# Kernel tuning notes

Hardware: AMD Instinct MI355X
Metric: run time of the kernel (lower is better)

## Reference

```python
import jax, jax.numpy as jnp
import numpy as np

BIT = 64
N_CLASS = 100
NUM_TRAIN = 100000
BATCH = 512
MU = 1.0   # config['mu']
M = 1.0    # config['m']
ETA = 0.5  # config['eta']
VUL = 1.0  # config['vul']
NTA = 1.0  # config['nta']


def setup_inputs() -> dict:
    key = jax.random.key(0)
    k1, k2, k3, k4, k5, k6 = jax.random.split(key, 6)
    u = jax.random.normal(k1, (BATCH, BIT), jnp.float32)
    # y / Y are one-hot label matrices in DFH; build realistic one-hot floats
    labels = jax.random.randint(k2, (BATCH,), 0, N_CLASS)
    y = jax.nn.one_hot(labels, N_CLASS, dtype=jnp.float32)
    ind = jax.random.randint(k3, (BATCH,), 0, NUM_TRAIN)
    U = jax.random.normal(k4, (BIT, NUM_TRAIN), jnp.float32)
    train_labels = jax.random.randint(k5, (NUM_TRAIN,), 0, N_CLASS)
    Y = jax.nn.one_hot(train_labels, N_CLASS, dtype=jnp.float32).T  # [n_class, num_train]
    V = jax.random.normal(k6, (BIT, N_CLASS), jnp.float32)
    return {"u": u, "y": y, "ind": ind, "U": U, "Y": Y, "V": V}


def _center_gradient(V, y, b):
    # 200-step gradient descent on V minimizing intra + vul*inter + nta*quant.
    n_class = V.shape[1]
    TK = V.shape[0] * (2.0 * jnp.eye(n_class, dtype=V.dtype)
                       - jnp.ones((n_class, n_class), V.dtype))
    yt = y.T  # [n_class, batch]

    def inner_loss(Vc):
        intra = jnp.mean((Vc @ yt - b) ** 2)
        inter = jnp.mean((Vc.T @ Vc - TK) ** 2)
        quant = jnp.mean((Vc - jnp.sign(Vc)) ** 2)
        return intra + VUL * inter + NTA * quant

    grad_fn = jax.grad(inner_loss)

    def step(Vc, i):
        # torch code multiplies alpha by 0.1 *before* the update at i==149 and i==179
        alpha = 0.03 * jnp.where(i >= 149, 0.1, 1.0) * jnp.where(i >= 179, 0.1, 1.0)
        return Vc - alpha * grad_fn(Vc), None

    V_new, _ = jax.lax.scan(step, V, jnp.arange(200))
    return V_new


def reference(u, y, ind, U, Y, V):
    # state buffer updates (torch: self.U[:, ind] = u.t().data, etc.)
    U = U.at[:, ind].set(u.T)
    Y = Y.at[:, ind].set(y.T)
    C = jnp.sign(V)
    b = jnp.sign(MU * (C @ y.T) + u.T)                     # [bit, batch]
    V_new = _center_gradient(V, y, b)                      # updated self.V
    s = (y @ Y > 0).astype(u.dtype)                        # [batch, num_train]
    ip = jnp.clip(0.5 * (u @ U), -100.0, 50.0)             # [batch, num_train]
    metric_loss = jnp.mean((1.0 - s) * jnp.log1p(jnp.exp(M + ip))
                           + s * jnp.log1p(jnp.exp(M - ip)))
    quantization_loss = jnp.mean((b - u.T) ** 2)
    loss = metric_loss + ETA * quantization_loss
    return loss, V_new
```

## Files before the change

### kernel.cpp

```cpp
#include <hip/hip_runtime.h>

#define BIT 64
#define NCLASS 100
#define NTRAIN 100000
#define BATCH 512

#define O_OWNER   0
#define O_LAB     200000
#define O_BMAT    200512
#define O_BSUM    233280
#define O_COUNT   239680
#define O_QSUM    239780
#define O_MSUM    239782

typedef __attribute__((ext_vector_type(8))) short short8v;
typedef __attribute__((ext_vector_type(4))) float f32x4;
typedef unsigned short ushortT;

__device__ __forceinline__ float signf(float x) {
    return (x > 0.f) ? 1.f : ((x < 0.f) ? -1.f : 0.f);
}

__device__ __forceinline__ unsigned cvtpk(float lo, float hi) {
    unsigned r;
    asm("v_cvt_pk_bf16_f32 %0, %1, %2" : "=v"(r) : "v"(lo), "v"(hi));
    return r;
}
__device__ __forceinline__ float dpp_x1(float x) {
    union { float f; int i; } v; v.f = x;
    v.i = __builtin_amdgcn_mov_dpp(v.i, 0xB1, 0xF, 0xF, false);
    return v.f;
}
__device__ __forceinline__ float dpp_x2(float x) {
    union { float f; int i; } v; v.f = x;
    v.i = __builtin_amdgcn_mov_dpp(v.i, 0x4E, 0xF, 0xF, false);
    return v.f;
}

__global__ void k_prep(const float* __restrict__ y, const int* __restrict__ ind,
                       int* owner, int* lab) {
    int b = threadIdx.x;
    const float* row = y + b * NCLASS;
    int best = 0;
    for (int c = 0; c < NCLASS; ++c)
        if (row[c] > 0.5f) best = c;
    lab[b] = best;
    atomicMax(&owner[ind[b]], b);
}

__global__ void k_b(const float* __restrict__ u, const float* __restrict__ V,
                    const int* __restrict__ lab, float* bmat, double* qsum) {
    int bb = threadIdx.x;
    int r  = blockIdx.x;
    int c = lab[bb];
    float v  = V[r * NCLASS + c];
    float uu = u[bb * BIT + r];
    float t  = signf(v) + uu;
    float bv = signf(t);
    bmat[r * BATCH + bb] = bv;
    float d = bv - uu;
    double q = (double)(d * d);
    for (int off = 32; off; off >>= 1) q += __shfl_down(q, off);
    __shared__ double wsum[8];
    int wid = threadIdx.x >> 6, lane = threadIdx.x & 63;
    if (lane == 0) wsum[wid] = q;
    __syncthreads();
    if (threadIdx.x == 0) {
        double s = 0;
        for (int w = 0; w < 8; ++w) s += wsum[w];
        atomicAdd(qsum, s);
    }
}

__global__ void k_bsum(const float* __restrict__ bmat, const int* __restrict__ lab,
                       float* Bsum, float* count) {
    __shared__ int slab[BATCH];
    for (int i = threadIdx.x; i < BATCH; i += blockDim.x) slab[i] = lab[i];
    __syncthreads();
    int idx = blockIdx.x * blockDim.x + threadIdx.x;
    if (idx < BIT * NCLASS) {
        int r = idx / NCLASS, c = idx % NCLASS;
        const float* br = bmat + r * BATCH;
        float s = 0.f;
        for (int bb = 0; bb < BATCH; ++bb)
            if (slab[bb] == c) s += br[bb];
        Bsum[idx] = s;
    }
    if (blockIdx.x == 0 && threadIdx.x < NCLASS) {
        int c = threadIdx.x, n = 0;
        for (int bb = 0; bb < BATCH; ++bb)
            if (slab[bb] == c) ++n;
        count[c] = (float)n;
    }
}

__global__ __launch_bounds__(512, 4) void k_main(
        const float* __restrict__ V, const float* __restrict__ Bsum,
        const float* __restrict__ count, const float* __restrict__ u,
        const float* __restrict__ U, const float* __restrict__ Y,
        const int* __restrict__ lab, const int* __restrict__ owner,
        double* msum, float* __restrict__ out) {
    __shared__ __align__(16) char smem[69888];

    if (blockIdx.x == 0) {
        ushortT* SAb = (ushortT*)smem;
        ushortT* SBb = (ushortT*)(smem + 32768);
        ushortT* SMf = (ushortT*)(smem + 61440);
        float*   rs  = (float*)(smem + 69632);

        const int t = threadIdx.x, l = t & 63, w = t >> 6;
        const int g = l >> 4, c16 = l & 15;
        const int h = w >> 2;
        const int mtile = w & 3;
        const int m = mtile * 16 + c16;
        const bool dg = ((mtile >> 1) == h);
        const short8v ONES = {0x3F80,0x3F80,0x3F80,0x3F80,
                              0x3F80,0x3F80,0x3F80,0x3F80};

        for (int i = t; i < 16384; i += 512) SAb[i] = 0;
        for (int i = t; i < 14336; i += 512) SBb[i] = 0;

        const float ci = 2.0f / 32768.0f;
        const float ce = 4.0f / 10000.0f;
        const float cq = 2.0f / 6400.0f;
        const float ce64 = 64.0f * ce;

        bool live[4];
        int sbO[4];
        float vreg[4][4], Kc[4][4], ncib[4][4];
        #pragma unroll
        for (int q = 0; q < 4; ++q) {
            const int nt = 4 * h + q;
            const int n0 = nt * 16 + 4 * g;
            const bool wact = (nt < 7);
            live[q] = wact && (n0 < NCLASS);
            sbO[q] = ((nt * 2 + (mtile >> 1)) * 64 +
                      (16 * (c16 >> 2) + 4 * g + (c16 & 3))) * 8 + 4 * (mtile & 1);
            #pragma unroll
            for (int r = 0; r < 4; ++r) {
                float v = 0.f, bs = 0.f, cn = 0.f;
                if (live[q]) {
                    const int n = n0 + r;
                    v  = V[m * NCLASS + n];
                    bs = Bsum[m * NCLASS + n];
                    cn = count[n];
                }
                vreg[q][r] = v;
                Kc[q][r]   = ci * cn + cq - 128.f * ce;
                ncib[q][r] = -ci * bs;
            }
        }
        const int saO0 = (mtile * 4 + 2 * h) * 512 + l * 8;
        const int saO1 = saO0 + 512;

        auto store_frags = [&](ushortT* SAn, ushortT* SBn) {
            uint4 wa;
            wa.x = cvtpk(vreg[0][0], vreg[0][1]);
            wa.y = cvtpk(vreg[0][2], vreg[0][3]);
            wa.z = cvtpk(vreg[1][0], vreg[1][1]);
            wa.w = cvtpk(vreg[1][2], vreg[1][3]);
            *(uint4*)&SAn[saO0] = wa;
            wa.x = cvtpk(vreg[2][0], vreg[2][1]);
            wa.y = cvtpk(vreg[2][2], vreg[2][3]);
            wa.z = cvtpk(vreg[3][0], vreg[3][1]);
            wa.w = cvtpk(vreg[3][2], vreg[3][3]);
            *(uint4*)&SAn[saO1] = wa;
            #pragma unroll
            for (int q = 0; q < 4; ++q) {
                if (4 * h + q < 7) {
                    float a0 = vreg[q][0], a1 = vreg[q][1];
                    float a2 = vreg[q][2], a3 = vreg[q][3];
                    float t0 = dpp_x1(a1), t1 = dpp_x1(a0);
                    float t2 = dpp_x1(a3), t3 = dpp_x1(a2);
                    const bool o1 = (l & 1);
                    float c0 = o1 ? t0 : a0;
                    float c1 = o1 ? a1 : t1;
                    float c2 = o1 ? t2 : a2;
                    float c3 = o1 ? a3 : t3;
                    float u0 = dpp_x2(c2), u1 = dpp_x2(c3);
                    float u2 = dpp_x2(c0), u3 = dpp_x2(c1);
                    const bool o2 = (l & 2);
                    float d0 = o2 ? u0 : c0;
                    float d1 = o2 ? u1 : c1;
                    float d2 = o2 ? c2 : u2;
                    float d3 = o2 ? c3 : u3;
                    uint2 wb;
                    wb.x = cvtpk(d0, d1);
                    wb.y = cvtpk(d2, d3);
                    *(uint2*)&SBn[sbO[q]] = wb;
                }
            }
        };

        __syncthreads();
        store_frags(SAb, SBb);
        __syncthreads();

        int cur = 0;
        for (int step = 0; step < 200; ++step) {
            float alpha = 0.03f;
            if (step >= 149) alpha *= 0.1f;
            if (step >= 179) alpha *= 0.1f;

            const ushortT* SAc = SAb + cur * 8192;

            f32x4 aM0 = {0.f,0.f,0.f,0.f}, aM1 = {0.f,0.f,0.f,0.f};
            f32x4 aR  = {0.f,0.f,0.f,0.f};
            #pragma unroll
            for (int ks = 0; ks < 4; ++ks) {
                short8v b  = *(const short8v*)&SAc[mtile * 2048 + ks * 512 + l * 8];
                short8v a0 = *(const short8v*)&SAc[(2 * h) * 2048 + ks * 512 + l * 8];
                short8v a1 = *(const short8v*)&SAc[(2 * h + 1) * 2048 + ks * 512 + l * 8];
                aM0 = __builtin_amdgcn_mfma_f32_16x16x32_bf16(a0, b, aM0, 0, 0, 0);
                aM1 = __builtin_amdgcn_mfma_f32_16x16x32_bf16(a1, b, aM1, 0, 0, 0);
                if (dg)
                    aR = __builtin_amdgcn_mfma_f32_16x16x32_bf16(b, ONES, aR, 0, 0, 0);
            }
            {
                uint4 sm;
                sm.x = cvtpk(aM0[0], aM0[1]);
                sm.y = cvtpk(aM0[2], aM0[3]);
                sm.z = cvtpk(aM1[0], aM1[1]);
                sm.w = cvtpk(aM1[2], aM1[3]);
                *(uint4*)&SMf[(mtile * 2 + h) * 512 + l * 8] = sm;
            }
            if (dg && c16 == 0)
                *(f32x4*)&rs[mtile * 16 + 4 * g] = aR;
            __syncthreads();

            const ushortT* SBc = SBb + cur * 7168;
            f32x4 p[4];
            #pragma unroll
            for (int q = 0; q < 4; ++q) p[q] = (f32x4){0.f,0.f,0.f,0.f};
            #pragma unroll
            for (int kb = 0; kb < 2; ++kb) {
                short8v bP = *(const short8v*)&SMf[(mtile * 2 + kb) * 512 + l * 8];
                #pragma unroll
                for (int q = 0; q < 4; ++q) {
                    if (4 * h + q < 7) {
                        short8v aP = *(const short8v*)
                            &SBc[((4 * h + q) * 2 + kb) * 512 + l * 8];
                        p[q] = __builtin_amdgcn_mfma_f32_16x16x32_bf16(aP, bP, p[q], 0, 0, 0);
                    }
                }
            }
            const float rsm = rs[m];

            #pragma unroll
            for (int q = 0; q < 4; ++q) {
                if (4 * h + q < 7) {
                    #pragma unroll
                    for (int r = 0; r < 4; ++r) {
                        const float v = vreg[q][r];
                        float t1 = __builtin_fmaf(Kc[q][r], v, ncib[q][r]);
                        t1 = __builtin_fmaf(ce,   p[q][r], t1);
                        t1 = __builtin_fmaf(ce64, rsm,     t1);
                        t1 -= __builtin_copysignf(cq, v);
                        float vn = __builtin_fmaf(-alpha, t1, v);
                        vreg[q][r] = live[q] ? vn : 0.f;
                    }
                }
            }
            store_frags(SAb + (cur ^ 1) * 8192, SBb + (cur ^ 1) * 7168);
            __syncthreads();
            cur ^= 1;
        }

        #pragma unroll
        for (int q = 0; q < 4; ++q) {
            if (live[q]) {
                const int n0 = (4 * h + q) * 16 + 4 * g;
                #pragma unroll
                for (int r = 0; r < 4; ++r)
                    out[1 + m * NCLASS + n0 + r] = vreg[q][r];
            }
        }
    } else {
        float*  ut   = (float*)smem;
        int*    slab = (int*)(smem + 34816);
        double* wsum = (double*)(smem + 36864);
        int*    tls  = (int*)(smem + 36928);

        const int t = threadIdx.x;
        const int jj = t & 255;
        const int j = (blockIdx.x - 1) * 256 + jj;
        const int half = t >> 8;
        const bool jok = (j < NTRAIN);
        slab[t] = lab[t];

        if (half == 0) {
            int tl = 0;
            if (jok) {
                for (int c = 0; c < NCLASS; ++c)
                    if (Y[(size_t)c * NTRAIN + j] > 0.5f) tl = c;
                int ow = owner[j];
                if (ow >= 0) tl = lab[ow];
            }
            tls[jj] = tl;
        }
        __syncthreads();
        const int tl = tls[jj];

        const float* colbase = U;
        size_t cstride = NTRAIN;
        if (jok) {
            int ow = owner[j];
            if (ow >= 0) { colbase = u + (size_t)ow * BIT; cstride = 1; }
            else         { colbase = U + j; }
        }

        float lsum = 0.f;
        for (int ch = 0; ch < 4; ++ch) {
            __syncthreads();
            for (int i = t; i < 8192; i += 512) {
                int buf = i >> 12, k = (i >> 6) & 63, r = i & 63;
                ut[buf * 4352 + r * 68 + k] = u[((buf * 4 + ch) * 64 + k) * BIT + r];
            }
            __syncthreads();

            if (jok) {
                const float* myut = ut + half * 4352;
                float acc[64];
                #pragma unroll
                for (int k = 0; k < 64; ++k) acc[k] = 0.f;
                #pragma unroll 2
                for (int r = 0; r < BIT; ++r) {
                    float Uv = colbase[(size_t)r * cstride];
                    const float* urow = &myut[r * 68];
                    #pragma unroll
                    for (int qq = 0; qq < 16; ++qq) {
                        float4 uv = *(const float4*)&urow[qq * 4];
                        acc[4 * qq + 0] += uv.x * Uv;
                        acc[4 * qq + 1] += uv.y * Uv;
                        acc[4 * qq + 2] += uv.z * Uv;
                        acc[4 * qq + 3] += uv.w * Uv;
                    }
                }
                const int b0 = (half * 4 + ch) * 64;
                #pragma unroll
                for (int k = 0; k < 64; ++k) {
                    float ip = fminf(fmaxf(0.5f * acc[k], -100.f), 50.f);
                    float x = (slab[b0 + k] == tl) ? (1.0f - ip) : (1.0f + ip);
                    lsum += fmaxf(x, 0.f) + __logf(1.f + __expf(-fabsf(x)));
                }
            }
        }

        double d = (double)lsum;
        for (int off = 32; off; off >>= 1) d += __shfl_down(d, off);
        const int wid = t >> 6, lane = t & 63;
        if (lane == 0) wsum[wid] = d;
        __syncthreads();
        if (t == 0) {
            double s = 0;
            for (int ww = 0; ww < 8; ++ww) s += wsum[ww];
            atomicAdd(msum, s);
        }
    }
}

__global__ void k_final(const double* __restrict__ msum,
                        const double* __restrict__ qsum, float* out) {
    if (threadIdx.x == 0) {
        double loss = (*msum) / ((double)BATCH * (double)NTRAIN)
                    + 0.5 * ((*qsum) / ((double)BIT * (double)BATCH));
        out[0] = (float)loss;
    }
}

extern "C" void kernel_launch(void* const* d_in, const int* in_sizes, int n_in,
                              void* d_out, int out_size, void* d_ws, size_t ws_size,
                              hipStream_t stream) {
    const float* u   = (const float*)d_in[0];
    const float* y   = (const float*)d_in[1];
    const int*   ind = (const int*)d_in[2];
    const float* U   = (const float*)d_in[3];
    const float* Y   = (const float*)d_in[4];
    const float* V   = (const float*)d_in[5];
    float* out = (float*)d_out;

    int*   wsI = (int*)d_ws;
    float* wsF = (float*)d_ws;
    int*   owner = wsI + O_OWNER;
    int*   lab   = wsI + O_LAB;
    float* bmat  = wsF + O_BMAT;
    float* Bsum  = wsF + O_BSUM;
    float* count = wsF + O_COUNT;
    double* qsum = (double*)(wsF + O_QSUM);
    double* msum = (double*)(wsF + O_MSUM);

    hipMemsetAsync(owner, 0xFF, NTRAIN * sizeof(int), stream);
    hipMemsetAsync(wsF + O_QSUM, 0, 4 * sizeof(float), stream);

    k_prep<<<1, 512, 0, stream>>>(y, ind, owner, lab);
    k_b<<<64, 512, 0, stream>>>(u, V, lab, bmat, qsum);
    k_bsum<<<25, 256, 0, stream>>>(bmat, lab, Bsum, count);
    k_main<<<1 + (NTRAIN + 255) / 256, 512, 0, stream>>>(
        V, Bsum, count, u, U, Y, lab, owner, msum, out);
    k_final<<<1, 64, 0, stream>>>(msum, qsum, out);
}
```

Baseline: 392.3 us.

## Fuse prep kernels and reuse register fragments in center-gradient loop

```diff
diff --git a/kernel.cpp b/kernel.cpp
--- a/kernel.cpp
+++ b/kernel.cpp
@@ -7,7 +7,6 @@
 
 #define O_OWNER   0
 #define O_LAB     200000
-#define O_BMAT    200512
 #define O_BSUM    233280
 #define O_COUNT   239680
 #define O_QSUM    239780
@@ -37,70 +36,61 @@
     return v.f;
 }
 
-__global__ void k_prep(const float* __restrict__ y, const int* __restrict__ ind,
-                       int* owner, int* lab) {
-    int b = threadIdx.x;
-    const float* row = y + b * NCLASS;
+__global__ __launch_bounds__(512) void k_pre(
+        const float* __restrict__ y, const int* __restrict__ ind,
+        const float* __restrict__ u, const float* __restrict__ V,
+        int* owner, int* lab, float* Bsum, float* count, double* qsum) {
+    __shared__ float srow[BATCH];
+    __shared__ int   labl[BATCH];
+    __shared__ double wq[8];
+    const int r = blockIdx.x;
+    const int bb = threadIdx.x;
+
+    const float* yrow = y + bb * NCLASS;
     int best = 0;
     for (int c = 0; c < NCLASS; ++c)
-        if (row[c] > 0.5f) best = c;
-    lab[b] = best;
-    atomicMax(&owner[ind[b]], b);
-}
-
-__global__ void k_b(const float* __restrict__ u, const float* __restrict__ V,
-                    const int* __restrict__ lab, float* bmat, double* qsum) {
-    int bb = threadIdx.x;
-    int r  = blockIdx.x;
-    int c = lab[bb];
-    float v  = V[r * NCLASS + c];
-    float uu = u[bb * BIT + r];
-    float t  = signf(v) + uu;
-    float bv = signf(t);
-    bmat[r * BATCH + bb] = bv;
-    float d = bv - uu;
+        if (yrow[c] > 0.5f) best = c;
+    labl[bb] = best;
+    if (r == 0) {
+        lab[bb] = best;
+        atomicMax(&owner[ind[bb]], bb);
+    }
+
+    const float v  = V[r * NCLASS + best];
+    const float uu = u[bb * BIT + r];
+    const float bv = signf(signf(v) + uu);
+    srow[bb] = bv;
+    const float d = bv - uu;
     double q = (double)(d * d);
     for (int off = 32; off; off >>= 1) q += __shfl_down(q, off);
-    __shared__ double wsum[8];
-    int wid = threadIdx.x >> 6, lane = threadIdx.x & 63;
-    if (lane == 0) wsum[wid] = q;
+    const int wid = bb >> 6, lane = bb & 63;
+    if (lane == 0) wq[wid] = q;
     __syncthreads();
-    if (threadIdx.x == 0) {
+    if (bb == 0) {
         double s = 0;
-        for (int w = 0; w < 8; ++w) s += wsum[w];
+        for (int w = 0; w < 8; ++w) s += wq[w];
         atomicAdd(qsum, s);
     }
-}
-
-__global__ void k_bsum(const float* __restrict__ bmat, const int* __restrict__ lab,
-                       float* Bsum, float* count) {
-    __shared__ int slab[BATCH];
-    for (int i = threadIdx.x; i < BATCH; i += blockDim.x) slab[i] = lab[i];
-    __syncthreads();
-    int idx = blockIdx.x * blockDim.x + threadIdx.x;
-    if (idx < BIT * NCLASS) {
-        int r = idx / NCLASS, c = idx % NCLASS;
-        const float* br = bmat + r * BATCH;
-        float s = 0.f;
-        for (int bb = 0; bb < BATCH; ++bb)
-            if (slab[bb] == c) s += br[bb];
-        Bsum[idx] = s;
+
+    if (bb < NCLASS) {
+        float s = 0.f; int n = 0;
+        for (int k = 0; k < BATCH; ++k) {
+            const bool hit = (labl[k] == bb);
+            s += hit ? srow[k] : 0.f;
+            n += hit;
+        }
+        Bsum[r * NCLASS + bb] = s;
+        if (r == 0) count[bb] = (float)n;
     }
-    if (blockIdx.x == 0 && threadIdx.x < NCLASS) {
-        int c = threadIdx.x, n = 0;
-        for (int bb = 0; bb < BATCH; ++bb)
-            if (slab[bb] == c) ++n;
-        count[c] = (float)n;
-    }
-}
-
-__global__ __launch_bounds__(512, 4) void k_main(
+}
+
+__global__ __launch_bounds__(512, 2) void k_main(
         const float* __restrict__ V, const float* __restrict__ Bsum,
         const float* __restrict__ count, const float* __restrict__ u,
         const float* __restrict__ U, const float* __restrict__ Y,
         const int* __restrict__ lab, const int* __restrict__ owner,
         double* msum, float* __restrict__ out) {
-    __shared__ __align__(16) char smem[69888];
+    __shared__ __align__(16) char smem[81920];
 
     if (blockIdx.x == 0) {
         ushortT* SAb = (ushortT*)smem;
@@ -125,15 +115,15 @@
         const float cq = 2.0f / 6400.0f;
         const float ce64 = 64.0f * ce;
 
-        bool live[4];
+        bool live[4], wact[4];
         int sbO[4];
         float vreg[4][4], Kc[4][4], ncib[4][4];
         #pragma unroll
         for (int q = 0; q < 4; ++q) {
             const int nt = 4 * h + q;
             const int n0 = nt * 16 + 4 * g;
-            const bool wact = (nt < 7);
-            live[q] = wact && (n0 < NCLASS);
+            wact[q] = (nt < 7);
+            live[q] = wact[q] && (n0 < NCLASS);
             sbO[q] = ((nt * 2 + (mtile >> 1)) * 64 +
                       (16 * (c16 >> 2) + 4 * g + (c16 & 3))) * 8 + 4 * (mtile & 1);
             #pragma unroll
@@ -153,21 +143,22 @@
         const int saO0 = (mtile * 4 + 2 * h) * 512 + l * 8;
         const int saO1 = saO0 + 512;
 
+        uint4 waA, waB;
+
         auto store_frags = [&](ushortT* SAn, ushortT* SBn) {
-            uint4 wa;
-            wa.x = cvtpk(vreg[0][0], vreg[0][1]);
-            wa.y = cvtpk(vreg[0][2], vreg[0][3]);
-            wa.z = cvtpk(vreg[1][0], vreg[1][1]);
-            wa.w = cvtpk(vreg[1][2], vreg[1][3]);
-            *(uint4*)&SAn[saO0] = wa;
-            wa.x = cvtpk(vreg[2][0], vreg[2][1]);
-            wa.y = cvtpk(vreg[2][2], vreg[2][3]);
-            wa.z = cvtpk(vreg[3][0], vreg[3][1]);
-            wa.w = cvtpk(vreg[3][2], vreg[3][3]);
-            *(uint4*)&SAn[saO1] = wa;
+            waA.x = cvtpk(vreg[0][0], vreg[0][1]);
+            waA.y = cvtpk(vreg[0][2], vreg[0][3]);
+            waA.z = cvtpk(vreg[1][0], vreg[1][1]);
+            waA.w = cvtpk(vreg[1][2], vreg[1][3]);
+            *(uint4*)&SAn[saO0] = waA;
+            waB.x = cvtpk(vreg[2][0], vreg[2][1]);
+            waB.y = cvtpk(vreg[2][2], vreg[2][3]);
+            waB.z = cvtpk(vreg[3][0], vreg[3][1]);
+            waB.w = cvtpk(vreg[3][2], vreg[3][3]);
+            *(uint4*)&SAn[saO1] = waB;
             #pragma unroll
             for (int q = 0; q < 4; ++q) {
-                if (4 * h + q < 7) {
+                if (wact[q]) {
                     float a0 = vreg[q][0], a1 = vreg[q][1];
                     float a2 = vreg[q][2], a3 = vreg[q][3];
                     float t0 = dpp_x1(a1), t1 = dpp_x1(a0);
@@ -203,52 +194,72 @@
             if (step >= 179) alpha *= 0.1f;
 
             const ushortT* SAc = SAb + cur * 8192;
+            const ushortT* SBc = SBb + cur * 7168;
+
+            short8v a0[4], a1[4], bx0, bx1;
+            #pragma unroll
+            for (int ks = 0; ks < 4; ++ks) {
+                a0[ks] = *(const short8v*)&SAc[(2 * h) * 2048 + ks * 512 + l * 8];
+                a1[ks] = *(const short8v*)&SAc[(2 * h + 1) * 2048 + ks * 512 + l * 8];
+            }
+            {
+                const int ko = 2 * (1 - h);
+                bx0 = *(const short8v*)&SAc[mtile * 2048 + ko * 512 + l * 8];
+                bx1 = *(const short8v*)&SAc[mtile * 2048 + (ko + 1) * 512 + l * 8];
+            }
+            short8v aP[4][2];
+            #pragma unroll
+            for (int q = 0; q < 4; ++q) {
+                if (wact[q]) {
+                    #pragma unroll
+                    for (int kb = 0; kb < 2; ++kb)
+                        aP[q][kb] = *(const short8v*)
+                            &SBc[((4 * h + q) * 2 + kb) * 512 + l * 8];
+                }
+            }
 
             f32x4 aM0 = {0.f,0.f,0.f,0.f}, aM1 = {0.f,0.f,0.f,0.f};
             f32x4 aR  = {0.f,0.f,0.f,0.f};
             #pragma unroll
             for (int ks = 0; ks < 4; ++ks) {
-                short8v b  = *(const short8v*)&SAc[mtile * 2048 + ks * 512 + l * 8];
-                short8v a0 = *(const short8v*)&SAc[(2 * h) * 2048 + ks * 512 + l * 8];
-                short8v a1 = *(const short8v*)&SAc[(2 * h + 1) * 2048 + ks * 512 + l * 8];
-                aM0 = __builtin_amdgcn_mfma_f32_16x16x32_bf16(a0, b, aM0, 0, 0, 0);
-                aM1 = __builtin_amdgcn_mfma_f32_16x16x32_bf16(a1, b, aM1, 0, 0, 0);
+                short8v b;
+                if (ks == 2 * h)          b = *(const short8v*)&waA;
+                else if (ks == 2 * h + 1) b = *(const short8v*)&waB;
+                else if (ks == 2 * (1 - h)) b = bx0;
+                else                        b = bx1;
+                aM0 = __builtin_amdgcn_mfma_f32_16x16x32_bf16(a0[ks], b, aM0, 0, 0, 0);
+                aM1 = __builtin_amdgcn_mfma_f32_16x16x32_bf16(a1[ks], b, aM1, 0, 0, 0);
                 if (dg)
                     aR = __builtin_amdgcn_mfma_f32_16x16x32_bf16(b, ONES, aR, 0, 0, 0);
             }
-            {
-                uint4 sm;
-                sm.x = cvtpk(aM0[0], aM0[1]);
-                sm.y = cvtpk(aM0[2], aM0[3]);
-                sm.z = cvtpk(aM1[0], aM1[1]);
-                sm.w = cvtpk(aM1[2], aM1[3]);
-                *(uint4*)&SMf[(mtile * 2 + h) * 512 + l * 8] = sm;
-            }
+            uint4 smpack;
+            smpack.x = cvtpk(aM0[0], aM0[1]);
+            smpack.y = cvtpk(aM0[2], aM0[3]);
+            smpack.z = cvtpk(aM1[0], aM1[1]);
+            smpack.w = cvtpk(aM1[2], aM1[3]);
+            *(uint4*)&SMf[(mtile * 2 + h) * 512 + l * 8] = smpack;
             if (dg && c16 == 0)
                 *(f32x4*)&rs[mtile * 16 + 4 * g] = aR;
             __syncthreads();
 
-            const ushortT* SBc = SBb + cur * 7168;
+            uint4 smo = *(const uint4*)&SMf[(mtile * 2 + (1 - h)) * 512 + l * 8];
+            const short8v bP0 = h ? *(const short8v*)&smo : *(const short8v*)&smpack;
+            const short8v bP1 = h ? *(const short8v*)&smpack : *(const short8v*)&smo;
             f32x4 p[4];
             #pragma unroll
             for (int q = 0; q < 4; ++q) p[q] = (f32x4){0.f,0.f,0.f,0.f};
             #pragma unroll
-            for (int kb = 0; kb < 2; ++kb) {
-                short8v bP = *(const short8v*)&SMf[(mtile * 2 + kb) * 512 + l * 8];
-                #pragma unroll
-                for (int q = 0; q < 4; ++q) {
-                    if (4 * h + q < 7) {
-                        short8v aP = *(const short8v*)
-                            &SBc[((4 * h + q) * 2 + kb) * 512 + l * 8];
-                        p[q] = __builtin_amdgcn_mfma_f32_16x16x32_bf16(aP, bP, p[q], 0, 0, 0);
-                    }
+            for (int q = 0; q < 4; ++q) {
+                if (wact[q]) {
+                    p[q] = __builtin_amdgcn_mfma_f32_16x16x32_bf16(aP[q][0], bP0, p[q], 0, 0, 0);
+                    p[q] = __builtin_amdgcn_mfma_f32_16x16x32_bf16(aP[q][1], bP1, p[q], 0, 0, 0);
                 }
             }
             const float rsm = rs[m];
 
             #pragma unroll
             for (int q = 0; q < 4; ++q) {
-                if (4 * h + q < 7) {
+                if (wact[q]) {
                     #pragma unroll
                     for (int r = 0; r < 4; ++r) {
                         const float v = vreg[q][r];
@@ -383,7 +394,6 @@
     float* wsF = (float*)d_ws;
     int*   owner = wsI + O_OWNER;
     int*   lab   = wsI + O_LAB;
-    float* bmat  = wsF + O_BMAT;
     float* Bsum  = wsF + O_BSUM;
     float* count = wsF + O_COUNT;
     double* qsum = (double*)(wsF + O_QSUM);
@@ -392,9 +402,7 @@
     hipMemsetAsync(owner, 0xFF, NTRAIN * sizeof(int), stream);
     hipMemsetAsync(wsF + O_QSUM, 0, 4 * sizeof(float), stream);
 
-    k_prep<<<1, 512, 0, stream>>>(y, ind, owner, lab);
-    k_b<<<64, 512, 0, stream>>>(u, V, lab, bmat, qsum);
-    k_bsum<<<25, 256, 0, stream>>>(bmat, lab, Bsum, count);
+    k_pre<<<64, 512, 0, stream>>>(y, ind, u, V, owner, lab, Bsum, count, qsum);
     k_main<<<1 + (NTRAIN + 255) / 256, 512, 0, stream>>>(
         V, Bsum, count, u, U, Y, lab, owner, msum, out);
     k_final<<<1, 64, 0, stream>>>(msum, qsum, out);
```

New measurement: 394.3 us. About the same (+0.5%).
